# Optimization experiments

Hardware: AMD Instinct MI355X
Metric: run time of the kernel (lower is better)

The kernel has to match this reference:

```python
import jax, jax.numpy as jnp
import numpy as np

B = 16384      # batch
C = 8          # confounder_num
D = 256        # input_dim
H0, H1 = 512, 256  # hiden_units


def setup_inputs() -> dict:
    key = jax.random.key(0)
    ks = jax.random.split(key, 8)
    s = lambda fan_in: 1.0 / np.sqrt(fan_in)
    x = jax.random.normal(ks[0], (B, D), dtype=jnp.float32)
    # per-confounder stacked weights: layer l weight [C, out, in]
    W0 = jax.random.uniform(ks[1], (C, H0, D), jnp.float32, -s(D), s(D))
    b0 = jax.random.uniform(ks[2], (C * H0,), jnp.float32, -s(D), s(D))
    W1 = jax.random.uniform(ks[3], (C, H1, H0), jnp.float32, -s(H0), s(H0))
    b1 = jax.random.uniform(ks[4], (C * H1,), jnp.float32, -s(H0), s(H0))
    W2 = jax.random.uniform(ks[5], (C, 1, H1), jnp.float32, -s(H1), s(H1))
    b2 = jax.random.uniform(ks[6], (C,), jnp.float32, -s(H1), s(H1))
    return {"x": x, "W0": W0, "b0": b0, "W1": W1, "b1": b1, "W2": W2, "b2": b2}


def reference(x, W0, b0, W1, b1, W2, b2):
    # Layer 0: cat(weights, dim=0) then F.linear == shared-input grouped GEMM.
    # h: [B, C, H0]
    h = jnp.einsum('bd,chd->bch', x, W0) + b0.reshape(C, H0)
    # Layer 1: block_diag grouped linear (no cross-group mixing).
    h = jax.nn.relu(h)
    h = jnp.einsum('bci,coi->bco', h, W1) + b1.reshape(C, H1)
    # Final per-group scalar head -> [B, C]
    h = jax.nn.relu(h)
    out = jnp.einsum('bci,coi->bco', h, W2)[:, :, 0] + b2
    return out
```

## Files before the change

### kernel.cpp

```cpp
#include <hip/hip_runtime.h>

#define BATCH 16384
#define CNUM  8
#define DIN   256
#define NH0   512
#define NH1   256

#define BT       64
#define BTM      128
#define NTMAIN   1024
#define NTHREADS 512

#define X_ELEMS  (BATCH * DIN)
#define W0_ELEMS (CNUM * NH0 * DIN)
#define W1_ELEMS (CNUM * NH1 * NH0)
#define WS_NEED  ((size_t)(X_ELEMS + W0_ELEMS + W1_ELEMS) * 2)

typedef __bf16 bf16x8 __attribute__((ext_vector_type(8)));
typedef __bf16 bf16x4 __attribute__((ext_vector_type(4)));
typedef float  f32x4  __attribute__((ext_vector_type(4)));
typedef float  f32x8  __attribute__((ext_vector_type(8)));

#define MFMA16(a, b, c) __builtin_amdgcn_mfma_f32_16x16x32_bf16((a), (b), (c), 0, 0, 0)

__global__ __launch_bounds__(256)
void cvt_bf16(const float* __restrict__ x, const float* __restrict__ W0,
              const float* __restrict__ W1, __bf16* __restrict__ ws) {
    const int i = blockIdx.x * 256 + threadIdx.x;
    const float* src;
    __bf16* dst;
    int off;
    if (i < X_ELEMS / 8)                 { src = x;  dst = ws;                        off = i * 8; }
    else if (i < (X_ELEMS + W0_ELEMS)/8) { src = W0; dst = ws + X_ELEMS;             off = (i - X_ELEMS/8) * 8; }
    else                                 { src = W1; dst = ws + X_ELEMS + W0_ELEMS;  off = (i - (X_ELEMS + W0_ELEMS)/8) * 8; }
    f32x8 v = *(const f32x8*)(src + off);
    bf16x8 r;
    #pragma unroll
    for (int j = 0; j < 8; ++j) r[j] = (__bf16)v[j];
    *(bf16x8*)(dst + off) = r;
}

__global__ __launch_bounds__(NTMAIN, 4)
void confounder_main(const __bf16* __restrict__ ws,
                     const float* __restrict__ b0,
                     const float* __restrict__ b1,
                     const float* __restrict__ W2,
                     const float* __restrict__ b2,
                     float* __restrict__ out) {
    __shared__ __align__(16) __bf16 h0s[BTM * NH0];
    __shared__ float red[16][BTM];
    __bf16* xs = h0s;

    const __bf16* xbf = ws;
    const __bf16* w0b = ws + X_ELEMS;
    const __bf16* w1b = ws + X_ELEMS + W0_ELEMS;

    const int c    = blockIdx.x & 7;
    const int mb   = blockIdx.x >> 3;
    const int row0 = mb * BTM;

    const int tid  = threadIdx.x;
    const int w    = tid >> 6;
    const int lane = tid & 63;
    const int l15  = lane & 15;
    const int l4   = lane >> 4;

    #pragma unroll
    for (int q = 0; q < 4; ++q) {
        const int p  = w * 4 + q;
        const int mt = p >> 3, kc = p & 7;
        bf16x8 v = *(const bf16x8*)(xbf + (size_t)(row0 + mt * 16 + l15) * DIN + kc * 32 + 8 * l4);
        *(bf16x8*)(xs + (p * 64 + lane) * 8) = v;
    }

    const __bf16* w0r = w0b + ((size_t)c * NH0 + w * 32 + l15) * DIN + 8 * l4;
    const __bf16* w1r = w1b + ((size_t)c * NH1 + w * 16 + l15) * NH0 + 8 * l4;

    bf16x8 a0 = *(const bf16x8*)(w0r);
    bf16x8 a1 = *(const bf16x8*)(w0r + 16 * DIN);
    __syncthreads();

    f32x4 acc0[2][8];
    #pragma unroll
    for (int at = 0; at < 2; ++at)
        #pragma unroll
        for (int bt = 0; bt < 8; ++bt)
            acc0[at][bt] = (f32x4){0.f, 0.f, 0.f, 0.f};

    #pragma unroll
    for (int ks = 0; ks < 8; ++ks) {
        bf16x8 na0 = a0, na1 = a1;
        if (ks < 7) {
            na0 = *(const bf16x8*)(w0r + (ks + 1) * 32);
            na1 = *(const bf16x8*)(w0r + 16 * DIN + (ks + 1) * 32);
        }
        __builtin_amdgcn_s_setprio(1);
        #pragma unroll
        for (int bt = 0; bt < 8; ++bt) {
            bf16x8 bx = *(const bf16x8*)(xs + ((bt * 8 + ks) * 64 + lane) * 8);
            acc0[0][bt] = MFMA16(a0, bx, acc0[0][bt]);
            acc0[1][bt] = MFMA16(a1, bx, acc0[1][bt]);
        }
        __builtin_amdgcn_s_setprio(0);
        a0 = na0; a1 = na1;
    }

    bf16x8 q0 = *(const bf16x8*)(w1r);

    __syncthreads();

    #pragma unroll
    for (int at = 0; at < 2; ++at) {
        const int nb = w * 32 + at * 16 + 4 * l4;
        const f32x4 b4 = *(const f32x4*)(b0 + c * NH0 + nb);
        const int sub = (at * 2 + (l4 >> 1)) * 128 + l15 * 8 + 4 * (l4 & 1);
        #pragma unroll
        for (int bt = 0; bt < 8; ++bt) {
            const int g = bt * 16 + w;
            bf16x4 pk;
            #pragma unroll
            for (int r = 0; r < 4; ++r) {
                float v = acc0[at][bt][r] + b4[r];
                v = v > 0.f ? v : 0.f;
                pk[r] = (__bf16)v;
            }
            *(bf16x4*)(&h0s[g * 512 + sub]) = pk;
        }
    }
    __syncthreads();

    f32x4 acc1[8];
    #pragma unroll
    for (int bt = 0; bt < 8; ++bt)
        acc1[bt] = (f32x4){0.f, 0.f, 0.f, 0.f};

    bf16x8 a = q0;
    #pragma unroll
    for (int ks = 0; ks < 16; ++ks) {
        bf16x8 na = a;
        if (ks < 15) na = *(const bf16x8*)(w1r + (ks + 1) * 32);
        __builtin_amdgcn_s_setprio(1);
        #pragma unroll
        for (int bt = 0; bt < 8; ++bt) {
            bf16x8 bh = *(const bf16x8*)(&h0s[((bt * 16 + ks) * 64 + lane) * 8]);
            acc1[bt] = MFMA16(a, bh, acc1[bt]);
        }
        __builtin_amdgcn_s_setprio(0);
        a = na;
    }

    float part[8] = {0.f, 0.f, 0.f, 0.f, 0.f, 0.f, 0.f, 0.f};
    {
        const int ob = w * 16 + 4 * l4;
        const f32x4 b1v = *(const f32x4*)(b1 + c * NH1 + ob);
        const f32x4 w2v = *(const f32x4*)(W2 + c * NH1 + ob);
        #pragma unroll
        for (int r = 0; r < 4; ++r) {
            #pragma unroll
            for (int bt = 0; bt < 8; ++bt) {
                float v = acc1[bt][r] + b1v[r];
                v = v > 0.f ? v : 0.f;
                part[bt] += v * w2v[r];
            }
        }
    }
    #pragma unroll
    for (int bt = 0; bt < 8; ++bt) {
        part[bt] += __shfl_xor(part[bt], 16, 64);
        part[bt] += __shfl_xor(part[bt], 32, 64);
    }
    if (l4 == 0) {
        #pragma unroll
        for (int bt = 0; bt < 8; ++bt)
            red[w][bt * 16 + l15] = part[bt];
    }
    __syncthreads();

    if (tid < BTM) {
        float s = 0.f;
        #pragma unroll
        for (int ww = 0; ww < 16; ++ww) s += red[ww][tid];
        s += b2[c];
        out[(size_t)(row0 + tid) * CNUM + c] = s;
    }
}

__device__ __forceinline__ bf16x8 ld_cvt8(const float* __restrict__ p) {
    f32x8 v = *(const f32x8*)p;
    bf16x8 r;
    #pragma unroll
    for (int i = 0; i < 8; ++i) r[i] = (__bf16)v[i];
    return r;
}

#define P0 (NH0 + 8)

__global__ __launch_bounds__(NTHREADS, 4)
void confounder_fused(const float* __restrict__ x,
                      const float* __restrict__ W0,
                      const float* __restrict__ b0,
                      const float* __restrict__ W1,
                      const float* __restrict__ b1,
                      const float* __restrict__ W2,
                      const float* __restrict__ b2,
                      float* __restrict__ out) {
    __shared__ __align__(16) __bf16 h0s[BT * P0];
    __shared__ float red[8][BT];

    const int c    = blockIdx.x & 7;
    const int mb   = blockIdx.x >> 3;
    const int row0 = mb * BT;
    const int tid  = threadIdx.x;
    const int w    = tid >> 6;
    const int lane = tid & 63;
    const int l15  = lane & 15;
    const int l4   = lane >> 4;

    f32x4 acc0[4][4];
    #pragma unroll
    for (int mt = 0; mt < 4; ++mt)
        #pragma unroll
        for (int nt = 0; nt < 4; ++nt)
            acc0[mt][nt] = (f32x4){0.f, 0.f, 0.f, 0.f};

    const float* xb  = x  + (size_t)(row0 + l15) * DIN + 8 * l4;
    const float* w0b = W0 + ((size_t)c * NH0 + w * 64 + l15) * DIN + 8 * l4;

    #pragma unroll
    for (int ks = 0; ks < DIN / 32; ++ks) {
        bf16x8 a[4];
        #pragma unroll
        for (int mt = 0; mt < 4; ++mt)
            a[mt] = ld_cvt8(xb + mt * 16 * DIN + ks * 32);
        #pragma unroll
        for (int nt = 0; nt < 4; ++nt) {
            bf16x8 bf = ld_cvt8(w0b + nt * 16 * DIN + ks * 32);
            #pragma unroll
            for (int mt = 0; mt < 4; ++mt)
                acc0[mt][nt] = __builtin_amdgcn_mfma_f32_16x16x32_bf16(a[mt], bf, acc0[mt][nt], 0, 0, 0);
        }
    }
    #pragma unroll
    for (int nt = 0; nt < 4; ++nt) {
        const int n    = (w * 4 + nt) * 16 + l15;
        const float bv = b0[c * NH0 + n];
        #pragma unroll
        for (int mt = 0; mt < 4; ++mt)
            #pragma unroll
            for (int r = 0; r < 4; ++r) {
                float v = acc0[mt][nt][r] + bv;
                v = v > 0.f ? v : 0.f;
                h0s[(mt * 16 + l4 * 4 + r) * P0 + n] = (__bf16)v;
            }
    }
    __syncthreads();

    f32x4 acc1[2][4];
    #pragma unroll
    for (int ot = 0; ot < 2; ++ot)
        #pragma unroll
        for (int nt = 0; nt < 4; ++nt)
            acc1[ot][nt] = (f32x4){0.f, 0.f, 0.f, 0.f};

    const float* w1b = W1 + ((size_t)c * NH1 + w * 32 + l15) * NH0 + 8 * l4;

    #pragma unroll
    for (int ks = 0; ks < NH0 / 32; ++ks) {
        bf16x8 a[2];
        #pragma unroll
        for (int ot = 0; ot < 2; ++ot)
            a[ot] = ld_cvt8(w1b + ot * 16 * NH0 + ks * 32);
        #pragma unroll
        for (int nt = 0; nt < 4; ++nt) {
            bf16x8 bf = *(const bf16x8*)(&h0s[(nt * 16 + l15) * P0 + ks * 32 + 8 * l4]);
            #pragma unroll
            for (int ot = 0; ot < 2; ++ot)
                acc1[ot][nt] = __builtin_amdgcn_mfma_f32_16x16x32_bf16(a[ot], bf, acc1[ot][nt], 0, 0, 0);
        }
    }

    float part[4] = {0.f, 0.f, 0.f, 0.f};
    #pragma unroll
    for (int ot = 0; ot < 2; ++ot)
        #pragma unroll
        for (int r = 0; r < 4; ++r) {
            const int o     = (2 * w + ot) * 16 + l4 * 4 + r;
            const float b1v = b1[c * NH1 + o];
            const float w2v = W2[c * NH1 + o];
            #pragma unroll
            for (int nt = 0; nt < 4; ++nt) {
                float v = acc1[ot][nt][r] + b1v;
                v = v > 0.f ? v : 0.f;
                part[nt] += v * w2v;
            }
        }
    #pragma unroll
    for (int nt = 0; nt < 4; ++nt) {
        part[nt] += __shfl_xor(part[nt], 16, 64);
        part[nt] += __shfl_xor(part[nt], 32, 64);
    }
    if (l4 == 0) {
        #pragma unroll
        for (int nt = 0; nt < 4; ++nt)
            red[w][nt * 16 + l15] = part[nt];
    }
    __syncthreads();

    if (tid < BT) {
        float s = 0.f;
        #pragma unroll
        for (int ww = 0; ww < 8; ++ww) s += red[ww][tid];
        s += b2[c];
        out[(size_t)(row0 + tid) * CNUM + c] = s;
    }
}

extern "C" void kernel_launch(void* const* d_in, const int* in_sizes, int n_in,
                              void* d_out, int out_size, void* d_ws, size_t ws_size,
                              hipStream_t stream) {
    const float* x  = (const float*)d_in[0];
    const float* W0 = (const float*)d_in[1];
    const float* b0 = (const float*)d_in[2];
    const float* W1 = (const float*)d_in[3];
    const float* b1 = (const float*)d_in[4];
    const float* W2 = (const float*)d_in[5];
    const float* b2 = (const float*)d_in[6];
    float* out = (float*)d_out;

    if (ws_size >= WS_NEED) {
        __bf16* ws = (__bf16*)d_ws;
        cvt_bf16<<<dim3((X_ELEMS + W0_ELEMS + W1_ELEMS) / 8 / 256), dim3(256), 0, stream>>>(x, W0, W1, ws);
        confounder_main<<<dim3((BATCH / BTM) * CNUM), dim3(NTMAIN), 0, stream>>>(ws, b0, b1, W2, b2, out);
    } else {
        confounder_fused<<<dim3((BATCH / BT) * CNUM), dim3(NTHREADS), 0, stream>>>(x, W0, b0, W1, b1, W2, b2, out);
    }
}
```

Measured before the change: 159.8 us.

## Retile warps as 8 N-slices by 2 M-halves for better register reuse

The per-warp tiling of both GEMM stages changes. Each of 16 warps previously covered all 128 batch rows and a thin N-slice. Now warps form an 8×2 grid, with each warp taking 64 (layer 0) or 32 (layer 1) output features over half the rows, so each LDS B-fragment load feeds 4 or 2 MFMAs. This cuts LDS read traffic per MFMA and shrinks the final reduction to 8 partials per row, at the cost of more weight-fragment registers per warp and doubled global weight reads per block.

After: 212.1 us. +32.8%, slower.

```diff
diff --git a/kernel.cpp b/kernel.cpp
--- a/kernel.cpp
+++ b/kernel.cpp
@@ -48,7 +48,7 @@
                      const float* __restrict__ b2,
                      float* __restrict__ out) {
     __shared__ __align__(16) __bf16 h0s[BTM * NH0];
-    __shared__ float red[16][BTM];
+    __shared__ float red[16][64];
     __bf16* xs = h0s;
 
     const __bf16* xbf = ws;
@@ -64,6 +64,8 @@
     const int lane = tid & 63;
     const int l15  = lane & 15;
     const int l4   = lane >> 4;
+    const int ns   = w >> 1;
+    const int mh   = w & 1;
 
     #pragma unroll
     for (int q = 0; q < 4; ++q) {
@@ -73,50 +75,60 @@
         *(bf16x8*)(xs + (p * 64 + lane) * 8) = v;
     }
 
-    const __bf16* w0r = w0b + ((size_t)c * NH0 + w * 32 + l15) * DIN + 8 * l4;
-    const __bf16* w1r = w1b + ((size_t)c * NH1 + w * 16 + l15) * NH0 + 8 * l4;
-
-    bf16x8 a0 = *(const bf16x8*)(w0r);
-    bf16x8 a1 = *(const bf16x8*)(w0r + 16 * DIN);
-    __syncthreads();
-
-    f32x4 acc0[2][8];
-    #pragma unroll
-    for (int at = 0; at < 2; ++at)
-        #pragma unroll
-        for (int bt = 0; bt < 8; ++bt)
+    const __bf16* w0r = w0b + ((size_t)c * NH0 + ns * 64 + l15) * DIN + 8 * l4;
+    const __bf16* w1r = w1b + ((size_t)c * NH1 + ns * 32 + l15) * NH0 + 8 * l4;
+
+    bf16x8 a[4];
+    #pragma unroll
+    for (int at = 0; at < 4; ++at)
+        a[at] = *(const bf16x8*)(w0r + at * 16 * DIN);
+    __syncthreads();
+
+    f32x4 acc0[4][4];
+    #pragma unroll
+    for (int at = 0; at < 4; ++at)
+        #pragma unroll
+        for (int bt = 0; bt < 4; ++bt)
             acc0[at][bt] = (f32x4){0.f, 0.f, 0.f, 0.f};
 
     #pragma unroll
     for (int ks = 0; ks < 8; ++ks) {
-        bf16x8 na0 = a0, na1 = a1;
+        bf16x8 na[4];
+        #pragma unroll
+        for (int at = 0; at < 4; ++at)
+            na[at] = a[at];
         if (ks < 7) {
-            na0 = *(const bf16x8*)(w0r + (ks + 1) * 32);
-            na1 = *(const bf16x8*)(w0r + 16 * DIN + (ks + 1) * 32);
+            #pragma unroll
+            for (int at = 0; at < 4; ++at)
+                na[at] = *(const bf16x8*)(w0r + at * 16 * DIN + (ks + 1) * 32);
         }
         __builtin_amdgcn_s_setprio(1);
         #pragma unroll
-        for (int bt = 0; bt < 8; ++bt) {
-            bf16x8 bx = *(const bf16x8*)(xs + ((bt * 8 + ks) * 64 + lane) * 8);
-            acc0[0][bt] = MFMA16(a0, bx, acc0[0][bt]);
-            acc0[1][bt] = MFMA16(a1, bx, acc0[1][bt]);
+        for (int bt = 0; bt < 4; ++bt) {
+            bf16x8 bx = *(const bf16x8*)(xs + (((mh * 4 + bt) * 8 + ks) * 64 + lane) * 8);
+            #pragma unroll
+            for (int at = 0; at < 4; ++at)
+                acc0[at][bt] = MFMA16(a[at], bx, acc0[at][bt]);
         }
         __builtin_amdgcn_s_setprio(0);
-        a0 = na0; a1 = na1;
+        #pragma unroll
+        for (int at = 0; at < 4; ++at)
+            a[at] = na[at];
     }
 
     bf16x8 q0 = *(const bf16x8*)(w1r);
-
-    __syncthreads();
-
-    #pragma unroll
-    for (int at = 0; at < 2; ++at) {
-        const int nb = w * 32 + at * 16 + 4 * l4;
+    bf16x8 q1 = *(const bf16x8*)(w1r + 16 * NH0);
+
+    __syncthreads();
+
+    #pragma unroll
+    for (int at = 0; at < 4; ++at) {
+        const int nb = ns * 64 + at * 16 + 4 * l4;
         const f32x4 b4 = *(const f32x4*)(b0 + c * NH0 + nb);
-        const int sub = (at * 2 + (l4 >> 1)) * 128 + l15 * 8 + 4 * (l4 & 1);
-        #pragma unroll
-        for (int bt = 0; bt < 8; ++bt) {
-            const int g = bt * 16 + w;
+        const int sub = ((at & 1) * 2 + (l4 >> 1)) * 128 + l15 * 8 + 4 * (l4 & 1);
+        #pragma unroll
+        for (int bt = 0; bt < 4; ++bt) {
+            const int g = (mh * 4 + bt) * 16 + ns * 2 + (at >> 1);
             bf16x4 pk;
             #pragma unroll
             for (int r = 0; r < 4; ++r) {
@@ -129,57 +141,65 @@
     }
     __syncthreads();
 
-    f32x4 acc1[8];
-    #pragma unroll
-    for (int bt = 0; bt < 8; ++bt)
-        acc1[bt] = (f32x4){0.f, 0.f, 0.f, 0.f};
-
-    bf16x8 a = q0;
+    f32x4 acc1[2][4];
+    #pragma unroll
+    for (int ot = 0; ot < 2; ++ot)
+        #pragma unroll
+        for (int bt = 0; bt < 4; ++bt)
+            acc1[ot][bt] = (f32x4){0.f, 0.f, 0.f, 0.f};
+
+    bf16x8 a0 = q0, a1 = q1;
     #pragma unroll
     for (int ks = 0; ks < 16; ++ks) {
-        bf16x8 na = a;
-        if (ks < 15) na = *(const bf16x8*)(w1r + (ks + 1) * 32);
+        bf16x8 na0 = a0, na1 = a1;
+        if (ks < 15) {
+            na0 = *(const bf16x8*)(w1r + (ks + 1) * 32);
+            na1 = *(const bf16x8*)(w1r + 16 * NH0 + (ks + 1) * 32);
+        }
         __builtin_amdgcn_s_setprio(1);
         #pragma unroll
-        for (int bt = 0; bt < 8; ++bt) {
-            bf16x8 bh = *(const bf16x8*)(&h0s[((bt * 16 + ks) * 64 + lane) * 8]);
-            acc1[bt] = MFMA16(a, bh, acc1[bt]);
+        for (int bt = 0; bt < 4; ++bt) {
+            bf16x8 bh = *(const bf16x8*)(&h0s[(((mh * 4 + bt) * 16 + ks) * 64 + lane) * 8]);
+            acc1[0][bt] = MFMA16(a0, bh, acc1[0][bt]);
+            acc1[1][bt] = MFMA16(a1, bh, acc1[1][bt]);
         }
         __builtin_amdgcn_s_setprio(0);
-        a = na;
-    }
-
-    float part[8] = {0.f, 0.f, 0.f, 0.f, 0.f, 0.f, 0.f, 0.f};
-    {
-        const int ob = w * 16 + 4 * l4;
+        a0 = na0; a1 = na1;
+    }
+
+    float part[4] = {0.f, 0.f, 0.f, 0.f};
+    #pragma unroll
+    for (int ot = 0; ot < 2; ++ot) {
+        const int ob = ns * 32 + ot * 16 + 4 * l4;
         const f32x4 b1v = *(const f32x4*)(b1 + c * NH1 + ob);
         const f32x4 w2v = *(const f32x4*)(W2 + c * NH1 + ob);
         #pragma unroll
         for (int r = 0; r < 4; ++r) {
             #pragma unroll
-            for (int bt = 0; bt < 8; ++bt) {
-                float v = acc1[bt][r] + b1v[r];
+            for (int bt = 0; bt < 4; ++bt) {
+                float v = acc1[ot][bt][r] + b1v[r];
                 v = v > 0.f ? v : 0.f;
                 part[bt] += v * w2v[r];
             }
         }
     }
     #pragma unroll
-    for (int bt = 0; bt < 8; ++bt) {
+    for (int bt = 0; bt < 4; ++bt) {
         part[bt] += __shfl_xor(part[bt], 16, 64);
         part[bt] += __shfl_xor(part[bt], 32, 64);
     }
     if (l4 == 0) {
         #pragma unroll
-        for (int bt = 0; bt < 8; ++bt)
+        for (int bt = 0; bt < 4; ++bt)
             red[w][bt * 16 + l15] = part[bt];
     }
     __syncthreads();
 
     if (tid < BTM) {
+        const int mh2 = tid >> 6, ml = tid & 63;
         float s = 0.f;
         #pragma unroll
-        for (int ww = 0; ww < 16; ++ww) s += red[ww][tid];
+        for (int n2 = 0; n2 < 8; ++n2) s += red[n2 * 2 + mh2][ml];
         s += b2[c];
         out[(size_t)(row0 + tid) * CNUM + c] = s;
     }
```

## Use 32x32x16 MFMA for layer-1 GEMM with split M/N wave tiling

Applied to the files above, without the earlier changes.

Layer 1 switches from 16x16x32 to 32x32x16 bf16 MFMA instructions. The 16 waves are split into 8 N-slices of 32 outputs by 2 M-halves of 64 rows, and the h0 LDS layout is reorganized to match the 32x32 B-operand fragment order. The larger MFMA tile is meant to raise arithmetic intensity per LDS read and cut the number of B-fragment loads. In exchange it doubles the K-loop length, changes the reduction layout, and adds register pressure from 16-wide accumulators.

New measurement: 187.6 us. +17.4%, slower.

```diff
diff --git a/kernel.cpp b/kernel.cpp
--- a/kernel.cpp
+++ b/kernel.cpp
@@ -20,8 +20,10 @@
 typedef __bf16 bf16x4 __attribute__((ext_vector_type(4)));
 typedef float  f32x4  __attribute__((ext_vector_type(4)));
 typedef float  f32x8  __attribute__((ext_vector_type(8)));
+typedef float  f32x16 __attribute__((ext_vector_type(16)));
 
 #define MFMA16(a, b, c) __builtin_amdgcn_mfma_f32_16x16x32_bf16((a), (b), (c), 0, 0, 0)
+#define MFMA32(a, b, c) __builtin_amdgcn_mfma_f32_32x32x16_bf16((a), (b), (c), 0, 0, 0)
 
 __global__ __launch_bounds__(256)
 void cvt_bf16(const float* __restrict__ x, const float* __restrict__ W0,
@@ -48,7 +50,7 @@
                      const float* __restrict__ b2,
                      float* __restrict__ out) {
     __shared__ __align__(16) __bf16 h0s[BTM * NH0];
-    __shared__ float red[16][BTM];
+    __shared__ float red[16][64];
     __bf16* xs = h0s;
 
     const __bf16* xbf = ws;
@@ -64,6 +66,10 @@
     const int lane = tid & 63;
     const int l15  = lane & 15;
     const int l4   = lane >> 4;
+    const int l31  = lane & 31;
+    const int l5   = lane >> 5;
+    const int ns   = w >> 1;
+    const int mh   = w & 1;
 
     #pragma unroll
     for (int q = 0; q < 4; ++q) {
@@ -74,7 +80,7 @@
     }
 
     const __bf16* w0r = w0b + ((size_t)c * NH0 + w * 32 + l15) * DIN + 8 * l4;
-    const __bf16* w1r = w1b + ((size_t)c * NH1 + w * 16 + l15) * NH0 + 8 * l4;
+    const __bf16* w1r = w1b + ((size_t)c * NH1 + ns * 32 + l31) * NH0 + 8 * l5;
 
     bf16x8 a0 = *(const bf16x8*)(w0r);
     bf16x8 a1 = *(const bf16x8*)(w0r + 16 * DIN);
@@ -113,10 +119,10 @@
     for (int at = 0; at < 2; ++at) {
         const int nb = w * 32 + at * 16 + 4 * l4;
         const f32x4 b4 = *(const f32x4*)(b0 + c * NH0 + nb);
-        const int sub = (at * 2 + (l4 >> 1)) * 128 + l15 * 8 + 4 * (l4 & 1);
+        const int ebase = (l15 + 32 * (l4 >> 1)) * 8 + 4 * (l4 & 1);
         #pragma unroll
         for (int bt = 0; bt < 8; ++bt) {
-            const int g = bt * 16 + w;
+            const int g = (bt >> 1) * 32 + w * 2 + at;
             bf16x4 pk;
             #pragma unroll
             for (int r = 0; r < 4; ++r) {
@@ -124,62 +130,64 @@
                 v = v > 0.f ? v : 0.f;
                 pk[r] = (__bf16)v;
             }
-            *(bf16x4*)(&h0s[g * 512 + sub]) = pk;
-        }
-    }
-    __syncthreads();
-
-    f32x4 acc1[8];
-    #pragma unroll
-    for (int bt = 0; bt < 8; ++bt)
-        acc1[bt] = (f32x4){0.f, 0.f, 0.f, 0.f};
+            *(bf16x4*)(&h0s[g * 512 + ebase + (bt & 1) * 128]) = pk;
+        }
+    }
+    __syncthreads();
+
+    f32x16 acc1[2];
+    #pragma unroll
+    for (int bt2 = 0; bt2 < 2; ++bt2)
+        #pragma unroll
+        for (int r = 0; r < 16; ++r)
+            acc1[bt2][r] = 0.f;
 
     bf16x8 a = q0;
     #pragma unroll
-    for (int ks = 0; ks < 16; ++ks) {
+    for (int ks = 0; ks < 32; ++ks) {
         bf16x8 na = a;
-        if (ks < 15) na = *(const bf16x8*)(w1r + (ks + 1) * 32);
+        if (ks < 31) na = *(const bf16x8*)(w1r + (ks + 1) * 16);
         __builtin_amdgcn_s_setprio(1);
         #pragma unroll
-        for (int bt = 0; bt < 8; ++bt) {
-            bf16x8 bh = *(const bf16x8*)(&h0s[((bt * 16 + ks) * 64 + lane) * 8]);
-            acc1[bt] = MFMA16(a, bh, acc1[bt]);
+        for (int bt2 = 0; bt2 < 2; ++bt2) {
+            bf16x8 bh = *(const bf16x8*)(h0s + (((mh * 2 + bt2) * 32 + ks) * 64 + lane) * 8);
+            acc1[bt2] = MFMA32(a, bh, acc1[bt2]);
         }
         __builtin_amdgcn_s_setprio(0);
         a = na;
     }
 
-    float part[8] = {0.f, 0.f, 0.f, 0.f, 0.f, 0.f, 0.f, 0.f};
-    {
-        const int ob = w * 16 + 4 * l4;
+    float part[2] = {0.f, 0.f};
+    #pragma unroll
+    for (int q = 0; q < 4; ++q) {
+        const int ob = ns * 32 + 8 * q + 4 * l5;
         const f32x4 b1v = *(const f32x4*)(b1 + c * NH1 + ob);
         const f32x4 w2v = *(const f32x4*)(W2 + c * NH1 + ob);
         #pragma unroll
-        for (int r = 0; r < 4; ++r) {
-            #pragma unroll
-            for (int bt = 0; bt < 8; ++bt) {
-                float v = acc1[bt][r] + b1v[r];
+        for (int bt2 = 0; bt2 < 2; ++bt2) {
+            #pragma unroll
+            for (int r = 0; r < 4; ++r) {
+                float v = acc1[bt2][q * 4 + r] + b1v[r];
                 v = v > 0.f ? v : 0.f;
-                part[bt] += v * w2v[r];
+                part[bt2] += v * w2v[r];
             }
         }
     }
     #pragma unroll
-    for (int bt = 0; bt < 8; ++bt) {
-        part[bt] += __shfl_xor(part[bt], 16, 64);
-        part[bt] += __shfl_xor(part[bt], 32, 64);
-    }
-    if (l4 == 0) {
-        #pragma unroll
-        for (int bt = 0; bt < 8; ++bt)
-            red[w][bt * 16 + l15] = part[bt];
+    for (int bt2 = 0; bt2 < 2; ++bt2)
+        part[bt2] += __shfl_xor(part[bt2], 32, 64);
+    if (l5 == 0) {
+        #pragma unroll
+        for (int bt2 = 0; bt2 < 2; ++bt2)
+            red[w][bt2 * 32 + l31] = part[bt2];
     }
     __syncthreads();
 
     if (tid < BTM) {
+        const int mh2 = tid >> 6, ml = tid & 63;
         float s = 0.f;
         #pragma unroll
-        for (int ww = 0; ww < 16; ++ww) s += red[ww][tid];
+        for (int n2 = 0; n2 < 8; ++n2) s += red[n2 * 2 + mh2][ml];
         s += b2[c];
         out[(size_t)(row0 + tid) * CNUM + c] = s;
     }
```
